# Kernel optimization log

Hardware: AMD Instinct MI355X
Metric: run time of the kernel (lower is better)

The kernel has to match this reference:

```python
import jax, jax.numpy as jnp
import numpy as np

NUM_HEADS = 32
HEAD_DIM = 128
NUM_KV_HEADS = 8
SCALE = 0.08838834764831845  # 1/sqrt(128)
SEQ_LEN = 2048


def setup_inputs() -> dict:
    key = jax.random.key(0)
    kq, kk, kv = jax.random.split(key, 3)
    q = jax.random.normal(kq, (SEQ_LEN, NUM_HEADS * HEAD_DIM), dtype=jnp.float32)
    k = jax.random.normal(kk, (SEQ_LEN, NUM_KV_HEADS * HEAD_DIM), dtype=jnp.float32)
    v = jax.random.normal(kv, (SEQ_LEN, NUM_KV_HEADS * HEAD_DIM), dtype=jnp.float32)
    return {"q": q, "k": k, "v": v}


def reference(q, k, v):
    S = q.shape[0]
    qh = q.reshape(S, NUM_HEADS, HEAD_DIM)            # [S, H, D]
    kh = k.reshape(S, NUM_KV_HEADS, HEAD_DIM)         # [S, KVH, D]
    vh = v.reshape(S, NUM_KV_HEADS, HEAD_DIM)
    # GQA: repeat_interleave along head dim
    expand = NUM_HEADS // NUM_KV_HEADS
    kh = jnp.repeat(kh, expand, axis=1)               # [S, H, D]
    vh = jnp.repeat(vh, expand, axis=1)
    scores = jnp.einsum('ihd,jhd->ihj', qh, kh) * SCALE  # [S, H, S]
    causal = jnp.triu(jnp.ones((S, S), dtype=bool), k=1)  # True above diagonal
    scores = jnp.where(causal[:, None, :], jnp.float32(-jnp.inf), scores)
    weights = jax.nn.softmax(scores, axis=-1)
    o = jnp.einsum('ihj,jhd->ihd', weights, vh)       # [S, H, D]
    return o.reshape(S, NUM_HEADS * HEAD_DIM)
```

## Files before the change

kernel.cpp:

```cpp
#include <hip/hip_runtime.h>


#define SEQ   2048
#define NH    32
#define NKV   8
#define HD    128
#define QLD   4096
#define KLD   1024
#define VT_HEAD (HD * SEQ)

typedef __attribute__((ext_vector_type(8))) __bf16 bf16x8;
typedef __attribute__((ext_vector_type(4))) __bf16 bf16x4;
typedef __attribute__((ext_vector_type(2))) __bf16 bf16x2;
typedef __attribute__((ext_vector_type(4))) float  f32x4;
typedef __attribute__((ext_vector_type(4))) short  s16x4;
typedef __attribute__((ext_vector_type(2))) unsigned int u32x2;

static __device__ __forceinline__ unsigned int pack2(float lo, float hi) {
  bf16x2 t; t[0] = (__bf16)lo; t[1] = (__bf16)hi;
  return __builtin_bit_cast(unsigned int, t);
}

static __device__ __forceinline__ f32x4 mfma16(bf16x4 a, u32x2 b, f32x4 c) {
#if __has_builtin(__builtin_amdgcn_mfma_f32_16x16x16bf16_1k)
  return __builtin_amdgcn_mfma_f32_16x16x16bf16_1k(
      __builtin_bit_cast(s16x4, a), __builtin_bit_cast(s16x4, b), c, 0, 0, 0);
#else
  asm volatile("v_mfma_f32_16x16x16_bf16 %0, %1, %2, %0"
               : "+v"(c) : "v"(a), "v"(b));
  return c;
#endif
}

__global__ void convert_k(const float* __restrict__ k, __bf16* __restrict__ kb) {
  const int i = (blockIdx.x * 256 + threadIdx.x) * 4;
  float4 v = *(const float4*)(k + i);
  bf16x4 b;
  b[0] = (__bf16)v.x; b[1] = (__bf16)v.y; b[2] = (__bf16)v.z; b[3] = (__bf16)v.w;
  *(bf16x4*)(kb + i) = b;
}

__global__ void transpose_v(const float* __restrict__ v, __bf16* __restrict__ vt) {
  __shared__ __bf16 TT[HD][72];
  const int kvh = blockIdx.y;
  const int kb  = blockIdx.x * 64;
  const int t   = threadIdx.x;
  {
    const int key = t >> 2, dq = t & 3;
    const float* vp = v + (size_t)(kb + key) * KLD + kvh * HD + dq * 32;
#pragma unroll
    for (int j = 0; j < 8; ++j) {
      float4 x = *(const float4*)(vp + j * 4);
      const int d = dq * 32 + j * 4;
      TT[d + 0][key] = (__bf16)x.x; TT[d + 1][key] = (__bf16)x.y;
      TT[d + 2][key] = (__bf16)x.z; TT[d + 3][key] = (__bf16)x.w;
    }
  }
  __syncthreads();
  {
    const int dim = t >> 1, kh = (t & 1) * 32;
    __bf16* op = vt + (size_t)kvh * VT_HEAD + (size_t)dim * SEQ + kb + kh;
#pragma unroll
    for (int j = 0; j < 8; ++j)
      *(bf16x4*)(op + j * 4) = *(const bf16x4*)&TT[dim][kh + j * 4];
  }
}

__global__ __launch_bounds__(256, 2)
void fa_kernel(const float* __restrict__ q, const __bf16* __restrict__ kg,
               const __bf16* __restrict__ vt, float* __restrict__ out) {
  __shared__ __bf16 KB[2][8192];
  __shared__ __bf16 VB[2][8192];

  const int head = blockIdx.x;
  const int yb   = blockIdx.y;
  const int qt   = (yb < 8) ? (15 - yb) : (yb - 8);
  const int kvh  = head >> 2;
  const int tid  = threadIdx.x;
  const int wave = tid >> 6;
  const int lane = tid & 63;
  const int l15  = lane & 15;
  const int quad = lane >> 4;
  const int h3   = l15 & 7;
  const int rw   = qt * 128 + wave * 32;

  constexpr float QS = 0.08838834764831845f * 1.4426950408889634f;

  bf16x8 qf[2][4];
#pragma unroll
  for (int sub = 0; sub < 2; ++sub) {
    const float* qp = q + (size_t)(rw + sub * 16 + l15) * QLD + head * HD + quad * 8;
#pragma unroll
    for (int c = 0; c < 4; ++c) {
      float4 a0 = *(const float4*)(qp + c * 32);
      float4 a1 = *(const float4*)(qp + c * 32 + 4);
      bf16x8 f;
      f[0] = (__bf16)(a0.x * QS); f[1] = (__bf16)(a0.y * QS);
      f[2] = (__bf16)(a0.z * QS); f[3] = (__bf16)(a0.w * QS);
      f[4] = (__bf16)(a1.x * QS); f[5] = (__bf16)(a1.y * QS);
      f[6] = (__bf16)(a1.z * QS); f[7] = (__bf16)(a1.w * QS);
      qf[sub][c] = f;
    }
  }

  int kgo[4], vgo[4];
#pragma unroll
  for (int j = 0; j < 4; ++j) {
    const int key = (wave * 4 + j) * 4 + (lane >> 4);
    const int c8  = (lane & 15) ^ (key & 7);
    kgo[j] = key * KLD + kvh * HD + c8 * 8;
    const int dim = (wave * 4 + j) * 8 + (lane >> 3);
    const int kc8 = (lane & 7) ^ (dim & 7);
    vgo[j] = kvh * VT_HEAD + dim * SEQ + kc8 * 8;
  }

  auto dma_tile = [&](int kbase, int buf) {
#pragma unroll
    for (int j = 0; j < 4; ++j)
      __builtin_amdgcn_global_load_lds(
          (const __attribute__((address_space(1))) unsigned int*)(kg + kbase * KLD + kgo[j]),
          (__attribute__((address_space(3))) unsigned int*)&KB[buf][(wave * 4 + j) * 512],
          16, 0, 0);
#pragma unroll
    for (int j = 0; j < 4; ++j)
      __builtin_amdgcn_global_load_lds(
          (const __attribute__((address_space(1))) unsigned int*)(vt + kbase + vgo[j]),
          (__attribute__((address_space(3))) unsigned int*)&VB[buf][(wave * 4 + j) * 512],
          16, 0, 0);
  };

  int kaddr[4], vaddr[4];
#pragma unroll
  for (int c = 0; c < 4; ++c)
    kaddr[c] = l15 * 256 + (((c * 4 + quad) ^ h3) * 16);
#pragma unroll
  for (int kt = 0; kt < 4; ++kt)
    vaddr[kt] = l15 * 128 + (((kt * 2 + (quad >> 1)) ^ h3) * 16) + (quad & 1) * 8;

  f32x4 acc[2][8];
  f32x4 lp[2];
#pragma unroll
  for (int sub = 0; sub < 2; ++sub) {
    lp[sub] = (f32x4){0.f, 0.f, 0.f, 0.f};
#pragma unroll
    for (int nt = 0; nt < 8; ++nt) acc[sub][nt] = (f32x4){0.f, 0.f, 0.f, 0.f};
  }

  const int ntiles = 2 * qt + 2;
  dma_tile(0, 0);
  __syncthreads();

  for (int t = 0; t < ntiles; ++t) {
    const int buf = t & 1;
    if (t + 1 < ntiles) dma_tile((t + 1) * 64, buf ^ 1);

    const char* Kb = (const char*)&KB[buf][0];
    const char* Vb = (const char*)&VB[buf][0];

    u32x2 pk[2][4];
#pragma unroll
    for (int nt = 0; nt < 4; ++nt) {
      bf16x8 kf[4];
#pragma unroll
      for (int c = 0; c < 4; ++c)
        kf[c] = *(const bf16x8*)(Kb + kaddr[c] + nt * 4096);
#pragma unroll
      for (int sub = 0; sub < 2; ++sub) {
        f32x4 s = (f32x4){0.f, 0.f, 0.f, 0.f};
#pragma unroll
        for (int c = 0; c < 4; ++c)
          s = __builtin_amdgcn_mfma_f32_16x16x32_bf16(kf[c], qf[sub][c], s, 0, 0, 0);
        if (t * 64 + 63 > rw + sub * 16) {
          const int key0  = t * 64 + nt * 16 + quad * 4;
          const int myrow = rw + sub * 16 + l15;
#pragma unroll
          for (int e = 0; e < 4; ++e)
            if (key0 + e > myrow) s[e] = -1e30f;
        }
        f32x4 p;
#pragma unroll
        for (int e = 0; e < 4; ++e) p[e] = __builtin_amdgcn_exp2f(s[e]);
        lp[sub] += p;
        u32x2 pkk;
        pkk.x = pack2(p[0], p[1]);
        pkk.y = pack2(p[2], p[3]);
        pk[sub][nt] = pkk;
      }
    }

#pragma unroll
    for (int kt = 0; kt < 4; ++kt) {
#pragma unroll
      for (int nt = 0; nt < 8; ++nt) {
        bf16x4 vf = *(const bf16x4*)(Vb + vaddr[kt] + nt * 2048);
#pragma unroll
        for (int sub = 0; sub < 2; ++sub)
          acc[sub][nt] = mfma16(vf, pk[sub][kt], acc[sub][nt]);
      }
    }
    __syncthreads();
  }

#pragma unroll
  for (int sub = 0; sub < 2; ++sub) {
    float ls = lp[sub][0] + lp[sub][1] + lp[sub][2] + lp[sub][3];
    ls += __shfl_xor(ls, 16);
    ls += __shfl_xor(ls, 32);
    const float inv = 1.0f / ls;
    float* op = out + (size_t)(rw + sub * 16 + l15) * QLD + head * HD + quad * 4;
#pragma unroll
    for (int nt = 0; nt < 8; ++nt) {
      f32x4 r = acc[sub][nt];
      float4 w = {r[0] * inv, r[1] * inv, r[2] * inv, r[3] * inv};
      *(float4*)(op + nt * 16) = w;
    }
  }
}

extern "C" void kernel_launch(void* const* d_in, const int* in_sizes, int n_in,
                              void* d_out, int out_size, void* d_ws, size_t ws_size,
                              hipStream_t stream) {
  const float* q = (const float*)d_in[0];
  const float* k = (const float*)d_in[1];
  const float* v = (const float*)d_in[2];
  float* o = (float*)d_out;
  __bf16* kbf = (__bf16*)d_ws;
  __bf16* vtb = (__bf16*)d_ws + (size_t)SEQ * KLD;
  convert_k<<<2048, 256, 0, stream>>>(k, kbf);
  transpose_v<<<dim3(32, 8), 256, 0, stream>>>(v, vtb);
  fa_kernel<<<dim3(32, 16), 256, 0, stream>>>(q, kbf, vtb, o);
}
```

Before: 164.7 us.

## Merge K/V prepasses, change K LDS swizzle, reorder causal tile schedule

```diff
diff --git a/kernel.cpp b/kernel.cpp
--- a/kernel.cpp
+++ b/kernel.cpp
@@ -19,6 +19,10 @@
 static __device__ __forceinline__ unsigned int pack2(float lo, float hi) {
   bf16x2 t; t[0] = (__bf16)lo; t[1] = (__bf16)hi;
   return __builtin_bit_cast(unsigned int, t);
+}
+
+static __device__ __forceinline__ int gk_sw(int key) {
+  return (key & 3) | (((key >> 1) & 3) << 2);
 }
 
 static __device__ __forceinline__ f32x4 mfma16(bf16x4 a, u32x2 b, f32x4 c) {
@@ -32,22 +36,24 @@
 #endif
 }
 
-__global__ void convert_k(const float* __restrict__ k, __bf16* __restrict__ kb) {
-  const int i = (blockIdx.x * 256 + threadIdx.x) * 4;
-  float4 v = *(const float4*)(k + i);
-  bf16x4 b;
-  b[0] = (__bf16)v.x; b[1] = (__bf16)v.y; b[2] = (__bf16)v.z; b[3] = (__bf16)v.w;
-  *(bf16x4*)(kb + i) = b;
-}
-
-__global__ void transpose_v(const float* __restrict__ v, __bf16* __restrict__ vt) {
+__global__ void prepass(const float* __restrict__ k, const float* __restrict__ v,
+                        __bf16* __restrict__ kb, __bf16* __restrict__ vt) {
+  if (blockIdx.x < 2048) {
+    const int i = (blockIdx.x * 256 + threadIdx.x) * 4;
+    float4 x = *(const float4*)(k + i);
+    bf16x4 b;
+    b[0] = (__bf16)x.x; b[1] = (__bf16)x.y; b[2] = (__bf16)x.z; b[3] = (__bf16)x.w;
+    *(bf16x4*)(kb + i) = b;
+    return;
+  }
   __shared__ __bf16 TT[HD][72];
-  const int kvh = blockIdx.y;
-  const int kb  = blockIdx.x * 64;
+  const int vb  = blockIdx.x - 2048;
+  const int kvh = vb >> 5;
+  const int kbse = (vb & 31) * 64;
   const int t   = threadIdx.x;
   {
     const int key = t >> 2, dq = t & 3;
-    const float* vp = v + (size_t)(kb + key) * KLD + kvh * HD + dq * 32;
+    const float* vp = v + (size_t)(kbse + key) * KLD + kvh * HD + dq * 32;
 #pragma unroll
     for (int j = 0; j < 8; ++j) {
       float4 x = *(const float4*)(vp + j * 4);
@@ -59,7 +65,7 @@
   __syncthreads();
   {
     const int dim = t >> 1, kh = (t & 1) * 32;
-    __bf16* op = vt + (size_t)kvh * VT_HEAD + (size_t)dim * SEQ + kb + kh;
+    __bf16* op = vt + (size_t)kvh * VT_HEAD + (size_t)dim * SEQ + kbse + kh;
 #pragma unroll
     for (int j = 0; j < 8; ++j)
       *(bf16x4*)(op + j * 4) = *(const bf16x4*)&TT[dim][kh + j * 4];
@@ -74,7 +80,7 @@
 
   const int head = blockIdx.x;
   const int yb   = blockIdx.y;
-  const int qt   = (yb < 8) ? (15 - yb) : (yb - 8);
+  const int qt   = (yb < 8) ? (15 - 2 * yb) : (14 - 2 * (yb - 8));
   const int kvh  = head >> 2;
   const int tid  = threadIdx.x;
   const int wave = tid >> 6;
@@ -107,11 +113,11 @@
 #pragma unroll
   for (int j = 0; j < 4; ++j) {
     const int key = (wave * 4 + j) * 4 + (lane >> 4);
-    const int c8  = (lane & 15) ^ (key & 7);
-    kgo[j] = key * KLD + kvh * HD + c8 * 8;
+    const int c   = (lane & 15) ^ gk_sw(key & 15);
+    kgo[j] = key * KLD + kvh * HD + c * 8;
     const int dim = (wave * 4 + j) * 8 + (lane >> 3);
-    const int kc8 = (lane & 7) ^ (dim & 7);
-    vgo[j] = kvh * VT_HEAD + dim * SEQ + kc8 * 8;
+    const int kc  = (lane & 7) ^ (dim & 7);
+    vgo[j] = kvh * VT_HEAD + dim * SEQ + kc * 8;
   }
 
   auto dma_tile = [&](int kbase, int buf) {
@@ -129,10 +135,11 @@
           16, 0, 0);
   };
 
+  const int gkl = gk_sw(l15);
   int kaddr[4], vaddr[4];
 #pragma unroll
   for (int c = 0; c < 4; ++c)
-    kaddr[c] = l15 * 256 + (((c * 4 + quad) ^ h3) * 16);
+    kaddr[c] = l15 * 256 + (((c * 4 + quad) ^ gkl) * 16);
 #pragma unroll
   for (int kt = 0; kt < 4; ++kt)
     vaddr[kt] = l15 * 128 + (((kt * 2 + (quad >> 1)) ^ h3) * 16) + (quad & 1) * 8;
@@ -226,7 +233,6 @@
   float* o = (float*)d_out;
   __bf16* kbf = (__bf16*)d_ws;
   __bf16* vtb = (__bf16*)d_ws + (size_t)SEQ * KLD;
-  convert_k<<<2048, 256, 0, stream>>>(k, kbf);
-  transpose_v<<<dim3(32, 8), 256, 0, stream>>>(v, vtb);
+  prepass<<<2048 + 256, 256, 0, stream>>>(k, v, kbf, vtb);
   fa_kernel<<<dim3(32, 16), 256, 0, stream>>>(q, kbf, vtb, o);
 }
```

New measurement: 175.6 us. +6.6%, slower.
